# Optimization experiments

Hardware: AMD Instinct MI355X
Metric: run time of the kernel (lower is better)

The kernel has to match this reference:

```python
import jax, jax.numpy as jnp
import numpy as np

B, S, D, H = 4, 2048, 1024, 16
DK = D // H
NEG = -1e9


def setup_inputs() -> dict:
    key = jax.random.key(0)
    ks = jax.random.split(key, 11)
    s = 1.0 / np.sqrt(D)
    inp = {
        "query": jax.random.normal(ks[0], (B, S, D), jnp.float32),
        "key": jax.random.normal(ks[1], (B, S, D), jnp.float32),
        "value": jax.random.normal(ks[2], (B, S, D), jnp.float32),
        # causal mask, broadcastable to [B, H, S, S]; 0 -> masked
        "mask": jnp.tril(jnp.ones((S, S), dtype=bool))[None, None],
        # torch Linear weights: [out, in], y = x @ W.T + b
        "Wq": jax.random.uniform(ks[3], (D, D), jnp.float32, -s, s),
        "bq": jax.random.uniform(ks[4], (D,), jnp.float32, -s, s),
        "Wk": jax.random.uniform(ks[5], (D, D), jnp.float32, -s, s),
        "bk": jax.random.uniform(ks[6], (D,), jnp.float32, -s, s),
        "Wv": jax.random.uniform(ks[7], (D, D), jnp.float32, -s, s),
        "bv": jax.random.uniform(ks[8], (D,), jnp.float32, -s, s),
        "Wo": jax.random.uniform(ks[9], (D, D), jnp.float32, -s, s),
        "bo": jax.random.uniform(ks[10], (D,), jnp.float32, -s, s),
    }
    return inp


def reference(query, key, value, mask, Wq, bq, Wk, bk, Wv, bv, Wo, bo):
    def proj(x, W, b):
        y = jnp.einsum('bsd,ed->bse', x, W) + b          # torch Linear: x @ W.T + b
        return y.reshape(B, S, H, DK).transpose(0, 2, 1, 3)  # [B, H, S, DK]

    Q = proj(query, Wq, bq)
    K = proj(key, Wk, bk)
    V = proj(value, Wv, bv)

    scale = 1.0 / np.sqrt(DK)
    scores = jnp.einsum('bhqd,bhkd->bhqk', Q, K) * scale  # [B, H, S, S]
    scores = jnp.where(mask, scores, NEG)
    attn = jax.nn.softmax(scores, axis=-1)
    out = jnp.einsum('bhqk,bhkd->bhqd', attn, V)          # [B, H, S, DK]
    out = out.transpose(0, 2, 1, 3).reshape(B, S, D)
    return jnp.einsum('bsd,ed->bse', out, Wo) + bo
```

## Files before the change

kernel.cpp:

```cpp
#include <hip/hip_runtime.h>
#include <stdint.h>

typedef __attribute__((ext_vector_type(8))) short bf16x8;
typedef __attribute__((ext_vector_type(4))) short s16x4;
typedef __attribute__((ext_vector_type(4))) float f32x4;
typedef __attribute__((ext_vector_type(16))) float f32x16;
typedef __attribute__((ext_vector_type(2))) unsigned u32x2;

#define DEVI __device__ __forceinline__

constexpr int B_ = 4, S_ = 2048, D_ = 1024, H_ = 16, DK_ = 64;
constexpr int M_ = B_ * S_;

DEVI short f2bf(float f) {
  union { float f; uint32_t u; } x; x.f = f;
  uint32_t r = x.u + 0x7fffu + ((x.u >> 16) & 1u);
  return (short)(uint16_t)(r >> 16);
}
DEVI float exp2_hw(float x) {
  float r; asm("v_exp_f32 %0, %1" : "=v"(r) : "v"(x)); return r;
}
DEVI uint32_t cvtpk(float lo, float hi) {
  uint32_t r; asm("v_cvt_pk_bf16_f32 %0, %1, %2" : "=v"(r) : "v"(lo), "v"(hi));
  return r;
}
#if __has_builtin(__builtin_amdgcn_permlane32_swap)
DEVI void plswap(uint32_t& a, uint32_t& b) {
  u32x2 r = __builtin_amdgcn_permlane32_swap(a, b, false, false);
  a = r[0]; b = r[1];
}
#else
DEVI void plswap(uint32_t& a, uint32_t& b) {
  const int h = (threadIdx.x & 63) >> 5;
  const uint32_t pa = (uint32_t)__shfl_xor((int)a, 32);
  const uint32_t pb = (uint32_t)__shfl_xor((int)b, 32);
  const uint32_t na = h ? pb : a;
  const uint32_t nb = h ? b : pa;
  a = na; b = nb;
}
#endif
DEVI void gload16(const short* g, short* l) {
  __builtin_amdgcn_global_load_lds((const __attribute__((address_space(1))) uint32_t*)g,
                                   (__attribute__((address_space(3))) uint32_t*)l, 16, 0, 0);
}

template <int LOG2G>
__global__ __launch_bounds__(256) void cvt3(const float* __restrict__ s0,
                                            const float* __restrict__ s1,
                                            const float* __restrict__ s2,
                                            const float* __restrict__ s3,
                                            short* __restrict__ d0,
                                            short* __restrict__ d1,
                                            short* __restrict__ d2,
                                            short* __restrict__ d3,
                                            int narr) {
  const int stride = gridDim.x * blockDim.x;
  const int total = narr << LOG2G;
  for (int g = blockIdx.x * blockDim.x + threadIdx.x; g < total; g += stride) {
    const int a = g >> LOG2G;
    const size_t off = (size_t)(g & ((1 << LOG2G) - 1)) * 8;
    const float* src = (a == 0) ? s0 : (a == 1) ? s1 : (a == 2) ? s2 : s3;
    short* dst = (a == 0) ? d0 : (a == 1) ? d1 : (a == 2) ? d2 : d3;
    const f32x4 x = *(const f32x4*)(src + off);
    const f32x4 y = *(const f32x4*)(src + off + 4);
    bf16x8 o;
#pragma unroll
    for (int e = 0; e < 4; ++e) { o[e] = f2bf(x[e]); o[e + 4] = f2bf(y[e]); }
    *(bf16x8*)(dst + off) = o;
  }
}

template <int MODE>
__global__ __launch_bounds__(512, 4) void gemm_bt(const short* __restrict__ A,
                                                  const short* __restrict__ Bw,
                                                  const float* __restrict__ bias,
                                                  void* __restrict__ Cout,
                                                  int Kdim, int Ndim, float scale) {
  __shared__ short sA[2][128 * 32];
  __shared__ short sB[2][128 * 32];
  const int tid = threadIdx.x;
  const int wid = tid >> 6, lane = tid & 63;
  const int m0 = blockIdx.x * 128, n0 = blockIdx.y * 128;
  const int wm = wid >> 1, wn = wid & 1;

  f32x4 acc[2][4];
#pragma unroll
  for (int i = 0; i < 2; ++i)
#pragma unroll
    for (int j = 0; j < 4; ++j) acc[i][j] = (f32x4){0.f, 0.f, 0.f, 0.f};

  const int srow = wid * 16 + (lane >> 2);
  const int swzs = (srow & 3) ^ ((srow >> 2) & 3);
  const int scol = ((lane & 3) ^ swzs) * 8;
  const short* gA = A + (size_t)(m0 + srow) * Kdim + scol;
  const short* gB = Bw + (size_t)(n0 + srow) * Kdim + scol;

  auto STAGE = [&](int bi, int kt) {
    gload16(gA + kt, &sA[bi][(wid * 16) * 32]);
    gload16(gB + kt, &sB[bi][(wid * 16) * 32]);
  };

  STAGE(0, 0);
  __syncthreads();
  int cur = 0;

  const int swzf = (lane & 3) ^ ((lane >> 2) & 3);
  const int cofs = (((lane >> 4) ^ swzf) << 3);

  for (int kt = 0; kt < Kdim; kt += 32) {
    if (kt + 32 < Kdim) STAGE(cur ^ 1, kt + 32);
    bf16x8 af[2], bfr[4];
#pragma unroll
    for (int mf = 0; mf < 2; ++mf)
      af[mf] = *(const bf16x8*)&sA[cur][(wm * 32 + mf * 16 + (lane & 15)) * 32 + cofs];
#pragma unroll
    for (int nf = 0; nf < 4; ++nf)
      bfr[nf] = *(const bf16x8*)&sB[cur][(wn * 64 + nf * 16 + (lane & 15)) * 32 + cofs];
#pragma unroll
    for (int mf = 0; mf < 2; ++mf)
#pragma unroll
      for (int nf = 0; nf < 4; ++nf)
        acc[mf][nf] = __builtin_amdgcn_mfma_f32_16x16x32_bf16(af[mf], bfr[nf], acc[mf][nf], 0, 0, 0);
    __syncthreads();
    cur ^= 1;
  }

#pragma unroll
  for (int mf = 0; mf < 2; ++mf) {
#pragma unroll
    for (int nf = 0; nf < 4; ++nf) {
      const int n = n0 + wn * 64 + nf * 16 + (lane & 15);
      const float bi = bias[n];
      if (MODE == 2) {
        const int m_base = m0 + wm * 32 + mf * 16 + ((lane >> 4) * 4);
        const int b = m_base >> 11, s0 = m_base & 2047;
        s16x4 pk;
#pragma unroll
        for (int r = 0; r < 4; ++r) pk[r] = f2bf(acc[mf][nf][r] + bi);
        *(s16x4*)((short*)Cout + ((size_t)(b * 1024 + n)) * 2048 + s0) = pk;
      } else {
#pragma unroll
        for (int r = 0; r < 4; ++r) {
          const int m = m0 + wm * 32 + mf * 16 + ((lane >> 4) * 4) + r;
          const float vv = (acc[mf][nf][r] + bi) * scale;
          if (MODE == 0)
            ((short*)Cout)[(size_t)m * Ndim + n] = f2bf(vv);
          else
            ((float*)Cout)[(size_t)m * Ndim + n] = vv;
        }
      }
    }
  }
}

__global__ __launch_bounds__(512, 4) void attn_fwd(const short* __restrict__ Qf,
                                                   const short* __restrict__ Kf,
                                                   const short* __restrict__ Vt,
                                                   short* __restrict__ AO) {
  __shared__ short sK[2][64 * 64];
  __shared__ short sV[2][64 * 64];

  const int tid = threadIdx.x, wid = tid >> 6, lane = tid & 63;
  const int h = lane >> 5, ql = lane & 31;
  const int cpx = gridDim.x >> 3;
  const int wg = ((int)blockIdx.x & 7) * cpx + ((int)blockIdx.x >> 3);
  const int bh = wg >> 3;
  const int pi = wg & 7;
  const int b = bh >> 4, hd = bh & 15;
  const int panel = (wid < 4) ? (15 - pi) : pi;
  const int qw = panel * 128 + (wid & 3) * 32;
  const int qg = qw + ql;
  const size_t rowbase = (size_t)b * S_ * D_ + (size_t)hd * DK_;
  const size_t vbase = (size_t)bh * 64 * S_;

  bf16x8 aQ[4];
  {
    const short* qp = Qf + rowbase + (size_t)qg * D_ + h * 8;
#pragma unroll
    for (int d = 0; d < 4; ++d) aQ[d] = *(const bf16x8*)(qp + d * 16);
  }

  f32x16 o0, o1;
#pragma unroll
  for (int i = 0; i < 16; ++i) { o0[i] = 0.f; o1[i] = 0.f; }
  float m_run = -1e30f, lsum = 0.f;

  const int srow8 = lane >> 3;
  const int schunk = ((lane & 7) ^ srow8) * 8;
  const short* gK = Kf + rowbase + (size_t)(wid * 8 + srow8) * D_ + schunk;
  const short* gV = Vt + vbase + (size_t)(wid * 8 + srow8) * S_ + schunk;

  auto STAGE = [&](int bufi, int kt) {
    gload16(gK + (size_t)kt * D_, &sK[bufi][(wid * 8) * 64]);
    gload16(gV + kt, &sV[bufi][(wid * 8) * 64]);
  };

  const int nt = 32 - 2 * pi;
  STAGE(0, 0);
  __syncthreads();
  int cur = 0;

  const int swz = ((ql & 7) << 3);

  for (int t = 0; t < nt; ++t) {
    const int kt = t * 64;
    if (t + 1 < nt) STAGE(cur ^ 1, kt + 64);
    if (kt <= qw + 31) {
      const short* bK = &sK[cur][0];
      const short* bV = &sV[cur][0];
      f32x16 p0, p1;
#pragma unroll
      for (int i = 0; i < 16; ++i) { p0[i] = 0.f; p1[i] = 0.f; }
      __builtin_amdgcn_s_setprio(1);
#pragma unroll
      for (int d = 0; d < 4; ++d) {
        const int co = ((d * 2 + h) << 3) ^ swz;
        bf16x8 k0 = *(const bf16x8*)&bK[ql * 64 + co];
        bf16x8 k1 = *(const bf16x8*)&bK[(32 + ql) * 64 + co];
        p0 = __builtin_amdgcn_mfma_f32_32x32x16_bf16(k0, aQ[d], p0, 0, 0, 0);
        p1 = __builtin_amdgcn_mfma_f32_32x32x16_bf16(k1, aQ[d], p1, 0, 0, 0);
      }
      __builtin_amdgcn_s_setprio(0);
      if (kt + 63 > qw) {
        const int qk = qg - kt;
#pragma unroll
        for (int i = 0; i < 16; ++i) {
          const int k0i = 8 * (i >> 2) + 4 * h + (i & 3);
          if (k0i > qk) p0[i] = -1e30f;
          if (k0i + 32 > qk) p1[i] = -1e30f;
        }
      }
      float tr[8];
#pragma unroll
      for (int i = 0; i < 8; ++i)
        tr[i] = fmaxf(fmaxf(p0[i], p0[i + 8]), fmaxf(p1[i], p1[i + 8]));
#pragma unroll
      for (int s = 4; s > 0; s >>= 1)
#pragma unroll
        for (int i = 0; i < s; ++i) tr[i] = fmaxf(tr[i], tr[i + s]);
      float mx = fmaxf(tr[0], __shfl_xor(tr[0], 32));
      if (mx > m_run + 8.f) {
        const float corr = exp2_hw(m_run - mx);
        m_run = mx;
        lsum *= corr;
#pragma unroll
        for (int i = 0; i < 16; ++i) { o0[i] *= corr; o1[i] *= corr; }
      }
#pragma unroll
      for (int i = 0; i < 16; ++i) {
        p0[i] = exp2_hw(p0[i] - m_run);
        p1[i] = exp2_hw(p1[i] - m_run);
      }
      float sr[8];
#pragma unroll
      for (int i = 0; i < 8; ++i) sr[i] = (p0[i] + p0[i + 8]) + (p1[i] + p1[i + 8]);
#pragma unroll
      for (int s = 4; s > 0; s >>= 1)
#pragma unroll
        for (int i = 0; i < s; ++i) sr[i] += sr[i + s];
      lsum += sr[0] + __shfl_xor(sr[0], 32);
      uint32_t cj[8], dj[8];
#pragma unroll
      for (int j = 0; j < 4; ++j) {
        cj[j]     = cvtpk(p0[4 * j], p0[4 * j + 1]);
        dj[j]     = cvtpk(p0[4 * j + 2], p0[4 * j + 3]);
        cj[4 + j] = cvtpk(p1[4 * j], p1[4 * j + 1]);
        dj[4 + j] = cvtpk(p1[4 * j + 2], p1[4 * j + 3]);
      }
      __builtin_amdgcn_s_setprio(1);
#pragma unroll
      for (int m = 0; m < 4; ++m) {
        uint32_t w0 = cj[2 * m], w2 = cj[2 * m + 1];
        plswap(w0, w2);
        uint32_t w1 = dj[2 * m], w3 = dj[2 * m + 1];
        plswap(w1, w3);
        union { uint32_t w[4]; bf16x8 v; } u;
        u.w[0] = w0; u.w[1] = w1; u.w[2] = w2; u.w[3] = w3;
        const int co = ((m * 2 + h) << 3) ^ swz;
        bf16x8 v0 = *(const bf16x8*)&bV[ql * 64 + co];
        bf16x8 v1 = *(const bf16x8*)&bV[(32 + ql) * 64 + co];
        o0 = __builtin_amdgcn_mfma_f32_32x32x16_bf16(v0, u.v, o0, 0, 0, 0);
        o1 = __builtin_amdgcn_mfma_f32_32x32x16_bf16(v1, u.v, o1, 0, 0, 0);
      }
      __builtin_amdgcn_s_setprio(0);
    }
    __syncthreads();
    cur ^= 1;
  }

  const float invl = 1.f / lsum;
  short* op = AO + rowbase + (size_t)qg * D_;
#pragma unroll
  for (int j = 0; j < 4; ++j) {
    s16x4 w0, w1;
#pragma unroll
    for (int r = 0; r < 4; ++r) {
      w0[r] = f2bf(o0[4 * j + r] * invl);
      w1[r] = f2bf(o1[4 * j + r] * invl);
    }
    *(s16x4*)(op + 8 * j + 4 * h) = w0;
    *(s16x4*)(op + 32 + 8 * j + 4 * h) = w1;
  }
}

extern "C" void kernel_launch(void* const* d_in, const int* in_sizes, int n_in,
                              void* d_out, int out_size, void* d_ws, size_t ws_size,
                              hipStream_t stream) {
  (void)in_sizes; (void)n_in; (void)out_size; (void)ws_size;
  const float* q  = (const float*)d_in[0];
  const float* k  = (const float*)d_in[1];
  const float* v  = (const float*)d_in[2];
  const float* Wq = (const float*)d_in[4];
  const float* bq = (const float*)d_in[5];
  const float* Wk = (const float*)d_in[6];
  const float* bk = (const float*)d_in[7];
  const float* Wv = (const float*)d_in[8];
  const float* bv = (const float*)d_in[9];
  const float* Wo = (const float*)d_in[10];
  const float* bo = (const float*)d_in[11];

  char* ws = (char*)d_ws;
  const size_t MB = 1ull << 20;
  short* wqb = (short*)(ws + 0 * MB);
  short* wkb = (short*)(ws + 2 * MB);
  short* wvb = (short*)(ws + 4 * MB);
  short* wob = (short*)(ws + 6 * MB);
  short* Qf  = (short*)(ws + 8 * MB);
  short* Kf  = (short*)(ws + 24 * MB);
  short* Vtb = (short*)(ws + 40 * MB);
  short* xq  = (short*)(ws + 56 * MB);
  short* xk  = (short*)(ws + 72 * MB);
  short* xv  = (short*)(ws + 88 * MB);
  short* AO  = xq;

  cvt3<20><<<2048, 256, 0, stream>>>(q, k, v, v, xq, xk, xv, xv, 3);
  cvt3<17><<<1024, 256, 0, stream>>>(Wq, Wk, Wv, Wo, wqb, wkb, wvb, wob, 4);

  dim3 gg(M_ / 128, D_ / 128);
  gemm_bt<0><<<gg, 512, 0, stream>>>(xq, wqb, bq, Qf, D_, D_, 0.125f * 1.4426950408889634f);
  gemm_bt<0><<<gg, 512, 0, stream>>>(xk, wkb, bk, Kf, D_, D_, 1.0f);
  gemm_bt<2><<<gg, 512, 0, stream>>>(xv, wvb, bv, Vtb, D_, D_, 1.0f);

  attn_fwd<<<dim3(512), 512, 0, stream>>>(Qf, Kf, Vtb, AO);

  gemm_bt<1><<<gg, 512, 0, stream>>>(AO, wob, bo, d_out, D_, D_, 1.0f);
}
```

Measured before the change: 200.1 us.

## Fuse Q/K/V projection GEMMs into one launch with 256-thread 4x4-fragment tiles

Replaces the three separate Q, K and V projection GEMM launches with a single gemm_qkv kernel that uses blockIdx.z to select the input, weight, bias and output layout. The new kernel runs 4 waves per 128x128 tile, each wave holding 4x4 MFMA fragments, instead of 8 waves with 2x4 fragments. This cuts two kernel launches, lets the three GEMMs share one grid for better load balance, and raises MFMA work per LDS fragment load. The cost is higher register pressure and fewer waves per block to hide latency. The MODE==2 transposed-V path is removed from gemm_bt.

```diff
diff --git a/kernel.cpp b/kernel.cpp
--- a/kernel.cpp
+++ b/kernel.cpp
@@ -70,6 +70,103 @@
   }
 }
 
+__global__ __launch_bounds__(256) void gemm_qkv(const short* __restrict__ xq,
+                                                const short* __restrict__ xk,
+                                                const short* __restrict__ xv,
+                                                const short* __restrict__ wq,
+                                                const short* __restrict__ wk,
+                                                const short* __restrict__ wv,
+                                                const float* __restrict__ bq,
+                                                const float* __restrict__ bk,
+                                                const float* __restrict__ bv,
+                                                short* __restrict__ Qf,
+                                                short* __restrict__ Kf,
+                                                short* __restrict__ Vt,
+                                                float scaleQ) {
+  __shared__ short sA[2][128 * 32];
+  __shared__ short sB[2][128 * 32];
+  const int z = blockIdx.z;
+  const short* A  = (z == 0) ? xq : (z == 1) ? xk : xv;
+  const short* Bw = (z == 0) ? wq : (z == 1) ? wk : wv;
+  const float* bias = (z == 0) ? bq : (z == 1) ? bk : bv;
+
+  const int tid = threadIdx.x;
+  const int wid = tid >> 6, lane = tid & 63;
+  const int m0 = blockIdx.x * 128, n0 = blockIdx.y * 128;
+  const int wm = wid >> 1, wn = wid & 1;
+
+  f32x4 acc[4][4];
+#pragma unroll
+  for (int i = 0; i < 4; ++i)
+#pragma unroll
+    for (int j = 0; j < 4; ++j) acc[i][j] = (f32x4){0.f, 0.f, 0.f, 0.f};
+
+  const int srow = wid * 32 + (lane >> 2);
+  const int swzs = (srow & 3) ^ ((srow >> 2) & 3);
+  const int scol = ((lane & 3) ^ swzs) * 8;
+  const short* gA = A + (size_t)(m0 + srow) * D_ + scol;
+  const short* gB = Bw + (size_t)(n0 + srow) * D_ + scol;
+
+  auto STAGE = [&](int bi, int kt) {
+    short* la = &sA[bi][(wid * 32) * 32];
+    short* lb = &sB[bi][(wid * 32) * 32];
+    gload16(gA + kt, la);
+    gload16(gA + (size_t)16 * D_ + kt, la + 16 * 32);
+    gload16(gB + kt, lb);
+    gload16(gB + (size_t)16 * D_ + kt, lb + 16 * 32);
+  };
+
+  STAGE(0, 0);
+  __syncthreads();
+  int cur = 0;
+
+  const int swzf = (lane & 3) ^ ((lane >> 2) & 3);
+  const int cofs = (((lane >> 4) ^ swzf) << 3);
+
+  for (int kt = 0; kt < D_; kt += 32) {
+    if (kt + 32 < D_) STAGE(cur ^ 1, kt + 32);
+    bf16x8 af[4], bfr[4];
+#pragma unroll
+    for (int mf = 0; mf < 4; ++mf)
+      af[mf] = *(const bf16x8*)&sA[cur][(wm * 64 + mf * 16 + (lane & 15)) * 32 + cofs];
+#pragma unroll
+    for (int nf = 0; nf < 4; ++nf)
+      bfr[nf] = *(const bf16x8*)&sB[cur][(wn * 64 + nf * 16 + (lane & 15)) * 32 + cofs];
+#pragma unroll
+    for (int mf = 0; mf < 4; ++mf)
+#pragma unroll
+      for (int nf = 0; nf < 4; ++nf)
+        acc[mf][nf] = __builtin_amdgcn_mfma_f32_16x16x32_bf16(af[mf], bfr[nf], acc[mf][nf], 0, 0, 0);
+    __syncthreads();
+    cur ^= 1;
+  }
+
+  const float scale = (z == 0) ? scaleQ : 1.0f;
+  short* Cout = (z == 0) ? Qf : Kf;
+#pragma unroll
+  for (int mf = 0; mf < 4; ++mf) {
+#pragma unroll
+    for (int nf = 0; nf < 4; ++nf) {
+      const int n = n0 + wn * 64 + nf * 16 + (lane & 15);
+      const float bi = bias[n];
+      if (z == 2) {
+        const int m_base = m0 + wm * 64 + mf * 16 + ((lane >> 4) * 4);
+        const int b = m_base >> 11, s0 = m_base & 2047;
+        s16x4 pk;
+#pragma unroll
+        for (int r = 0; r < 4; ++r) pk[r] = f2bf(acc[mf][nf][r] + bi);
+        *(s16x4*)(Vt + ((size_t)(b * 1024 + n)) * 2048 + s0) = pk;
+      } else {
+#pragma unroll
+        for (int r = 0; r < 4; ++r) {
+          const int m = m0 + wm * 64 + mf * 16 + ((lane >> 4) * 4) + r;
+          Cout[(size_t)m * D_ + n] = f2bf((acc[mf][nf][r] + bi) * scale);
+        }
+      }
+    }
+  }
+}
+
 template <int MODE>
 __global__ __launch_bounds__(512, 4) void gemm_bt(const short* __restrict__ A,
                                                   const short* __restrict__ Bw,
@@ -131,23 +228,14 @@
     for (int nf = 0; nf < 4; ++nf) {
       const int n = n0 + wn * 64 + nf * 16 + (lane & 15);
       const float bi = bias[n];
-      if (MODE == 2) {
-        const int m_base = m0 + wm * 32 + mf * 16 + ((lane >> 4) * 4);
-        const int b = m_base >> 11, s0 = m_base & 2047;
-        s16x4 pk;
-#pragma unroll
-        for (int r = 0; r < 4; ++r) pk[r] = f2bf(acc[mf][nf][r] + bi);
-        *(s16x4*)((short*)Cout + ((size_t)(b * 1024 + n)) * 2048 + s0) = pk;
-      } else {
-#pragma unroll
-        for (int r = 0; r < 4; ++r) {
-          const int m = m0 + wm * 32 + mf * 16 + ((lane >> 4) * 4) + r;
-          const float vv = (acc[mf][nf][r] + bi) * scale;
-          if (MODE == 0)
-            ((short*)Cout)[(size_t)m * Ndim + n] = f2bf(vv);
-          else
-            ((float*)Cout)[(size_t)m * Ndim + n] = vv;
-        }
+#pragma unroll
+      for (int r = 0; r < 4; ++r) {
+        const int m = m0 + wm * 32 + mf * 16 + ((lane >> 4) * 4) + r;
+        const float vv = (acc[mf][nf][r] + bi) * scale;
+        if (MODE == 0)
+          ((short*)Cout)[(size_t)m * Ndim + n] = f2bf(vv);
+        else
+          ((float*)Cout)[(size_t)m * Ndim + n] = vv;
       }
     }
   }
@@ -336,12 +424,11 @@
   cvt3<20><<<2048, 256, 0, stream>>>(q, k, v, v, xq, xk, xv, xv, 3);
   cvt3<17><<<1024, 256, 0, stream>>>(Wq, Wk, Wv, Wo, wqb, wkb, wvb, wob, 4);
 
-  dim3 gg(M_ / 128, D_ / 128);
-  gemm_bt<0><<<gg, 512, 0, stream>>>(xq, wqb, bq, Qf, D_, D_, 0.125f * 1.4426950408889634f);
-  gemm_bt<0><<<gg, 512, 0, stream>>>(xk, wkb, bk, Kf, D_, D_, 1.0f);
-  gemm_bt<2><<<gg, 512, 0, stream>>>(xv, wvb, bv, Vtb, D_, D_, 1.0f);
+  gemm_qkv<<<dim3(M_ / 128, D_ / 128, 3), 256, 0, stream>>>(
+      xq, xk, xv, wqb, wkb, wvb, bq, bk, bv, Qf, Kf, Vtb,
+      0.125f * 1.4426950408889634f);
 
   attn_fwd<<<dim3(512), 512, 0, stream>>>(Qf, Kf, Vtb, AO);
 
-  gemm_bt<1><<<gg, 512, 0, stream>>>(AO, wob, bo, d_out, D_, D_, 1.0f);
-}
+  gemm_bt<1><<<dim3(M_ / 128, D_ / 128), 512, 0, stream>>>(AO, wob, bo, d_out, D_, D_, 1.0f);
+}
```

Result: faster. 189.0 us (-5.6%).
